# Performance work log

Hardware: AMD Instinct MI355X
Metric: run time of the kernel (lower is better)

## Reference

```python
import jax, jax.numpy as jnp
import numpy as np

N_PP = 100000   # papers
N_A = 50000     # authors
N_AP = N_PP + N_A
DIM = 16
B = 8192        # sampled node set sizes
E = 500000      # edges per modality
ALPHA = 0.5
EPS = 1e-12


def _cdist(x, y):
    # Euclidean cdist via quadratic expansion (avoids [N,M,d] intermediate)
    sq = (jnp.sum(x * x, -1)[:, None] + jnp.sum(y * y, -1)[None, :]
          - 2.0 * x @ y.T)
    return jnp.sqrt(jnp.maximum(sq, EPS))


def _pdist(x, y):
    d = x - y
    return jnp.sqrt(jnp.sum(d * d, -1) + EPS)


def setup_inputs() -> dict:
    key = jax.random.key(0)
    ks = jax.random.split(key, 10)
    u = lambda k, s: jax.random.uniform(k, s, jnp.float32, -1.0, 1.0)  # 2*rand-1
    p = u(ks[0], (N_PP, DIM))
    p_star = u(ks[1], (N_PP, DIM))
    a = u(ks[2], (N_A, DIM))
    beta_ap = u(ks[3], (N_AP,))
    gamma_pp = u(ks[4], (2 * N_PP,))
    edges_pp = jax.random.randint(ks[5], (2, E), 0, N_PP, jnp.int32)
    e_ap0 = jax.random.randint(ks[6], (1, E), 0, N_PP, jnp.int32)
    e_ap1 = jax.random.randint(ks[7], (1, E), N_PP, N_AP, jnp.int32)
    edges_ap = jnp.concatenate([e_ap0, e_ap1], 0)
    p_star_nodes = jnp.sort(jax.random.randint(ks[8], (B,), 0, N_PP, jnp.int32))
    kk = jax.random.split(ks[9], 2)
    p_nodes = jax.random.randint(kk[0], (B,), 0, N_PP, jnp.int32)
    a_nodes = jax.random.randint(kk[1], (B,), N_PP, N_AP, jnp.int32)
    return {"p": p, "p_star": p_star, "a": a, "beta_ap": beta_ap,
            "gamma_pp": gamma_pp, "edges_pp": edges_pp, "edges_ap": edges_ap,
            "p_star_nodes": p_star_nodes, "p_nodes": p_nodes, "a_nodes": a_nodes}


def reference(p, p_star, a, beta_ap, gamma_pp,
              edges_pp, edges_ap, p_star_nodes, p_nodes, a_nodes):
    # ---- pp modality ----
    # link term over edges (edges[0]=p_star idx, edges[1]=p idx)
    link_pp = jnp.sum(gamma_pp[edges_pp[0]] + gamma_pp[edges_pp[1] + N_PP]
                      - _pdist(p_star[edges_pp[0]], p[edges_pp[1]]))
    # non-link term: [B_pstar, B_p] matrix, upper-triangular (k=1) masked sum
    g_ps = gamma_pp[p_star_nodes]                 # [B]
    g_p = gamma_pp[p_nodes + N_PP]                # [B]
    mat_pp = g_ps[:, None] + g_p[None, :]         # == gamma_mat.T in torch code
    dist_pp = _cdist(p_star[p_star_nodes], p[p_nodes])
    nonlink_pp = jnp.sum(jnp.triu(jnp.exp(mat_pp - dist_pp), k=1))
    nll_pp = -(link_pp - nonlink_pp)

    # ---- ap modality ----
    link_ap = jnp.sum(beta_ap[edges_ap[0]] + beta_ap[edges_ap[1]]
                      - _pdist(p_star[edges_ap[0]], a[edges_ap[1] - N_PP]))
    b_ps = beta_ap[p_star_nodes]
    b_a = beta_ap[a_nodes]
    mat_ap = b_ps[:, None] + b_a[None, :]         # == beta_mat.T
    dist_ap = _cdist(p_star[p_star_nodes], a[a_nodes - N_PP])
    nonlink_ap = jnp.sum(jnp.exp(mat_ap - dist_ap))
    nll_ap = -(link_ap - nonlink_ap)

    # average batch loss as in __train_one_batch
    loss = ALPHA * nll_pp / B + (1.0 - ALPHA) * nll_ap / B
    return loss
```

## Files before the change

### kernel.cpp

```cpp
#include <hip/hip_runtime.h>

#define N_PP 100000
#define N_A  50000
#define N_AP 150000
#define NEDGE 500000
#define BSZ 8192
#define TILE 128
#define SCALE 1.44269504088896f
#define QSI4 (1.0f / 7.0f)

#define EB 977
#define GRID_P 2048
#define PP_JOBS 2080
#define AP_JOBS 4096
#define PJOBS (PP_JOBS + AP_JOBS)

#define GRID_FB 2048

typedef __attribute__((ext_vector_type(8)))  short bf16x8;
typedef __attribute__((ext_vector_type(16))) float f32x16;
typedef __attribute__((ext_vector_type(4)))  float f32x4;
typedef unsigned short u16;

#if __has_builtin(__builtin_amdgcn_sqrtf)
#define FAST_SQRT(x) __builtin_amdgcn_sqrtf(x)
#else
#define FAST_SQRT(x) sqrtf(x)
#endif
#if __has_builtin(__builtin_amdgcn_exp2f)
#define FAST_EXP2(x) __builtin_amdgcn_exp2f(x)
#else
#define FAST_EXP2(x) exp2f(x)
#endif

__device__ __forceinline__ u16 f2bf(float f) {
    unsigned u = __builtin_bit_cast(unsigned, f);
    u += 0x7FFFu + ((u >> 16) & 1u);
    return (u16)(u >> 16);
}
__device__ __forceinline__ float bf2f(u16 s) {
    unsigned u = ((unsigned)s) << 16;
    return __builtin_bit_cast(float, u);
}

__device__ __forceinline__ bf16x8 load_frag_f32(const float* __restrict__ src) {
    float4 v0 = *(const float4*)src;
    float4 v1 = *(const float4*)(src + 4);
    bf16x8 f;
    f[0] = (short)f2bf(v0.x); f[1] = (short)f2bf(v0.y);
    f[2] = (short)f2bf(v0.z); f[3] = (short)f2bf(v0.w);
    f[4] = (short)f2bf(v1.x); f[5] = (short)f2bf(v1.y);
    f[6] = (short)f2bf(v1.z); f[7] = (short)f2bf(v1.w);
    return f;
}

__device__ __forceinline__ float dist_i4q(int2 ra, int2 rb) {
    int d2 = 0;
#pragma unroll
    for (int c = 0; c < 8; ++c) {
        int va = (ra.x << (28 - 4 * c)) >> 28;
        int vb = (rb.x << (28 - 4 * c)) >> 28;
        int d = va - vb; d2 += d * d;
        int wa = (ra.y << (28 - 4 * c)) >> 28;
        int wb = (rb.y << (28 - 4 * c)) >> 28;
        int e = wa - wb; d2 += e * e;
    }
    return FAST_SQRT((float)d2) * QSI4;
}

__device__ __forceinline__ unsigned packq4x8(const float* __restrict__ v) {
    unsigned r = 0;
#pragma unroll
    for (int c = 0; c < 8; ++c) {
        int q = (int)rintf(v[c] * 7.0f);
        r |= ((unsigned)(q & 0xF)) << (4 * c);
    }
    return r;
}

__device__ __forceinline__ float pdist16_f32(const float* __restrict__ xv,
                                             const float* __restrict__ yv) {
    float d2 = 1e-12f;
#pragma unroll
    for (int c = 0; c < 16; c += 4) {
        float4 xq = *(const float4*)(xv + c);
        float4 yq = *(const float4*)(yv + c);
        float dx = xq.x - yq.x; d2 = fmaf(dx, dx, d2);
        float dy = xq.y - yq.y; d2 = fmaf(dy, dy, d2);
        float dz = xq.z - yq.z; d2 = fmaf(dz, dz, d2);
        float dw = xq.w - yq.w; d2 = fmaf(dw, dw, d2);
    }
    return sqrtf(d2);
}

__global__ __launch_bounds__(256) void prep_kernel(
        const float* __restrict__ p, const float* __restrict__ p_star,
        const float* __restrict__ a, const float* __restrict__ beta,
        const float* __restrict__ gamma,
        const int* __restrict__ psn, const int* __restrict__ pn,
        const int* __restrict__ an,
        int2* __restrict__ ps4, int2* __restrict__ p4, int2* __restrict__ a4,
        u16* __restrict__ gamma_h, u16* __restrict__ beta_h,
        u16* __restrict__ Xb, u16* __restrict__ Yp, u16* __restrict__ Ya,
        float* __restrict__ Xxx, float* __restrict__ Xg,
        float* __restrict__ Pyy, float* __restrict__ Pg,
        float* __restrict__ Ayy, float* __restrict__ Ag)
{
    const int NROWS = 250000;
    const int NBATCH = 3 * BSZ;
    const int NW = 2 * N_PP + N_AP;
    const int NITEMS = NROWS + NBATCH + NW;
    for (int i = blockIdx.x * 256 + threadIdx.x; i < NITEMS; i += gridDim.x * 256) {
        if (i < NROWS) {
            const float* src; int2* dst;
            if (i < 100000)      { src = p_star + (size_t)i * 16;       dst = ps4 + i; }
            else if (i < 200000) { src = p + (size_t)(i - 100000) * 16; dst = p4 + (i - 100000); }
            else                 { src = a + (size_t)(i - 200000) * 16; dst = a4 + (i - 200000); }
            float buf[16];
            *(float4*)(buf + 0)  = *(const float4*)(src + 0);
            *(float4*)(buf + 4)  = *(const float4*)(src + 4);
            *(float4*)(buf + 8)  = *(const float4*)(src + 8);
            *(float4*)(buf + 12) = *(const float4*)(src + 12);
            int2 q;
            q.x = (int)packq4x8(buf);
            q.y = (int)packq4x8(buf + 8);
            *dst = q;
        } else if (i < NROWS + NBATCH) {
            const int j = i - NROWS;
            const int which = j >> 13;
            const int r = j & (BSZ - 1);
            const float* src; float wsc; u16* drow; float* xxp; float* gp;
            if (which == 0) {
                int node = psn[r]; src = p_star + (size_t)node * 16;
                wsc = gamma[node] * SCALE; drow = Xb + (size_t)r * 16; xxp = Xxx; gp = Xg;
            } else if (which == 1) {
                int node = pn[r]; src = p + (size_t)node * 16;
                wsc = gamma[node + N_PP] * SCALE; drow = Yp + (size_t)r * 16; xxp = Pyy; gp = Pg;
            } else {
                int node = an[r]; src = a + (size_t)(node - N_PP) * 16;
                wsc = beta[node] * SCALE; drow = Ya + (size_t)r * 16; xxp = Ayy; gp = Ag;
            }
            bf16x8 lo = load_frag_f32(src);
            bf16x8 hi = load_frag_f32(src + 8);
            *(bf16x8*)drow = lo;
            *(bf16x8*)(drow + 8) = hi;
            float ss = 0.f;
#pragma unroll
            for (int c = 0; c < 8; ++c) {
                float q0 = bf2f((u16)lo[c]); ss = fmaf(q0, q0, ss);
                float q1 = bf2f((u16)hi[c]); ss = fmaf(q1, q1, ss);
            }
            xxp[r] = ss;
            gp[r] = wsc;
        } else {
            const int j = i - NROWS - NBATCH;
            if (j < 2 * N_PP) gamma_h[j] = f2bf(gamma[j]);
            else              beta_h[j - 2 * N_PP] = f2bf(beta[j - 2 * N_PP]);
        }
    }
}

template <bool DIAG>
__device__ __forceinline__ float epi_rt(
        const f32x16& ca, const f32x16& cb,
        const float* __restrict__ xxg, const float* __restrict__ gxg,
        int rb, float yy0, float gy0, float yy1, float gy1,
        int cj0, int cj1)
{
    f32x4 xxq[4], gxq[4];
#pragma unroll
    for (int q = 0; q < 4; ++q) {
        xxq[q] = *(const f32x4*)&xxg[rb + q * 8];
        gxq[q] = *(const f32x4*)&gxg[rb + q * 8];
    }
    float s = 0.f;
#pragma unroll
    for (int q = 0; q < 4; ++q) {
#pragma unroll
        for (int j = 0; j < 4; ++j) {
            const int reg = q * 4 + j;
            float sxy = xxq[q][j];
            float gx  = gxq[q][j];
            float sq0 = fmaf(-2.f, ca[reg], sxy + yy0);
            float d0  = FAST_SQRT(fmaxf(sq0, 1e-12f));
            float v0  = FAST_EXP2(fmaf(-SCALE, d0, gx + gy0));
            float sq1 = fmaf(-2.f, cb[reg], sxy + yy1);
            float d1  = FAST_SQRT(fmaxf(sq1, 1e-12f));
            float v1  = FAST_EXP2(fmaf(-SCALE, d1, gx + gy1));
            if (DIAG) {
                int row = rb + q * 8 + j;
                v0 = (cj0 > row) ? v0 : 0.f;
                v1 = (cj1 > row) ? v1 : 0.f;
            }
            s += v0 + v1;
        }
    }
    return s;
}

__device__ __forceinline__ void decode_job(int j, int& bx, int& by, bool& pp) {
    pp = (j < PP_JOBS);
    if (pp) {
        int k = j;
        float disc = sqrtf((float)(129 * 129 - 8 * k));
        by = (int)((129.0f - disc) * 0.5f);
        while (64 * by - (by * (by - 1)) / 2 > k) --by;
        while (64 * (by + 1) - ((by + 1) * by) / 2 <= k) ++by;
        bx = by + (k - (64 * by - (by * (by - 1)) / 2));
    } else {
        int k = j - PP_JOBS;
        bx = k & 63; by = k >> 6;
    }
}

__device__ __forceinline__ void load_pair_frags(
        int bx, int by, bool pp,
        const u16* __restrict__ Xb, const u16* __restrict__ Yp,
        const u16* __restrict__ Ya,
        int wr, int wc, int l31, int h,
        bf16x8& aF0, bf16x8& aF1, bf16x8& bF0, bf16x8& bF1)
{
    const u16* Ytab = pp ? Yp : Ya;
    const int ar0 = by * TILE + wr * 64 + l31;
    const int bc0 = bx * TILE + wc * 64 + l31;
    aF0 = *(const bf16x8*)(Xb   + (size_t)ar0 * 16 + h * 8);
    aF1 = *(const bf16x8*)(Xb   + (size_t)(ar0 + 32) * 16 + h * 8);
    bF0 = *(const bf16x8*)(Ytab + (size_t)bc0 * 16 + h * 8);
    bF1 = *(const bf16x8*)(Ytab + (size_t)(bc0 + 32) * 16 + h * 8);
}

__global__ __launch_bounds__(256) void work_kernel(
        const int* __restrict__ edges_pp, const int* __restrict__ edges_ap,
        const int2* __restrict__ ps4, const int2* __restrict__ p4,
        const int2* __restrict__ a4,
        const u16* __restrict__ gamma_h, const u16* __restrict__ beta_h,
        const u16* __restrict__ Xb, const u16* __restrict__ Yp,
        const u16* __restrict__ Ya,
        const float* __restrict__ Xxx, const float* __restrict__ Xg,
        const float* __restrict__ Pyy, const float* __restrict__ Pg,
        const float* __restrict__ Ayy, const float* __restrict__ Ag,
        float* __restrict__ epart, float* __restrict__ ppart)
{
    const int b = blockIdx.x;
    const int t = threadIdx.x;
    const int l = t & 63, w = t >> 6;

    if ((b % 3 == 0) && (b / 3 < EB)) {
        const int base = (b / 3) * 512;
        const int i0 = base + t;
        const int i1raw = base + 256 + t;
        const bool v1 = (i1raw < NEDGE);
        const int i1 = v1 ? i1raw : 0;

        int e0a = __builtin_nontemporal_load(edges_pp + i0);
        int e1a = __builtin_nontemporal_load(edges_pp + NEDGE + i0);
        int f0a = __builtin_nontemporal_load(edges_ap + i0);
        int f1a = __builtin_nontemporal_load(edges_ap + NEDGE + i0);
        int e0b = __builtin_nontemporal_load(edges_pp + i1);
        int e1b = __builtin_nontemporal_load(edges_pp + NEDGE + i1);
        int f0b = __builtin_nontemporal_load(edges_ap + i1);
        int f1b = __builtin_nontemporal_load(edges_ap + NEDGE + i1);

        int2 rA0 = ps4[e0a];
        int2 rA1 = p4[e1a];
        int2 rB0 = ps4[f0a];
        int2 rB1 = a4[f1a - N_PP];
        int2 rC0 = ps4[e0b];
        int2 rC1 = p4[e1b];
        int2 rD0 = ps4[f0b];
        int2 rD1 = a4[f1b - N_PP];
        float wA = bf2f(gamma_h[e0a]) + bf2f(gamma_h[e1a + N_PP]);
        float wB = bf2f(beta_h[f0a])  + bf2f(beta_h[f1a]);
        float wC = bf2f(gamma_h[e0b]) + bf2f(gamma_h[e1b + N_PP]);
        float wD = bf2f(beta_h[f0b])  + bf2f(beta_h[f1b]);

        float sppl = wA - dist_i4q(rA0, rA1);
        float sapl = wB - dist_i4q(rB0, rB1);
        float tpp2 = wC - dist_i4q(rC0, rC1);
        float tap2 = wD - dist_i4q(rD0, rD1);
        sppl += v1 ? tpp2 : 0.f;
        sapl += v1 ? tap2 : 0.f;

        __shared__ float rede[4][2];
#pragma unroll
        for (int o = 32; o > 0; o >>= 1) {
            sppl += __shfl_down(sppl, o, 64);
            sapl += __shfl_down(sapl, o, 64);
        }
        if (l == 0) { rede[w][0] = sppl; rede[w][1] = sapl; }
        __syncthreads();
        if (t < 2)
            epart[(size_t)(b / 3) * 2 + t] =
                rede[0][t] + rede[1][t] + rede[2][t] + rede[3][t];
        return;
    }

    const int pid = (b < 3 * EB) ? (b - b / 3 - 1) : (b - EB);

    const int wr = w >> 1, wc = w & 1;
    const int l31 = l & 31, h = l >> 5;
    const int cj0 = wc * 64 + l31, cj1 = cj0 + 32;
    const int rb0 = wr * 64 + 4 * h, rb1 = rb0 + 32;

    float s_ppn = 0.f, s_apn = 0.f;

    int j = pid;
    int bx, by; bool pp;
    bf16x8 aF0, aF1, bF0, bF1;
    if (j < PJOBS) {
        decode_job(j, bx, by, pp);
        load_pair_frags(bx, by, pp, Xb, Yp, Ya, wr, wc, l31, h, aF0, aF1, bF0, bF1);
    }

    while (j < PJOBS) {
        const int jn = j + GRID_P;
        int bxn, byn; bool ppn;
        bf16x8 nA0, nA1, nB0, nB1;
        const bool have_next = (jn < PJOBS);
        if (have_next) {
            decode_job(jn, bxn, byn, ppn);
            load_pair_frags(bxn, byn, ppn, Xb, Yp, Ya, wr, wc, l31, h, nA0, nA1, nB0, nB1);
        }

        const bool diag = pp && (bx == by);
        const float* yyP = (pp ? Pyy : Ayy) + bx * TILE;
        const float* gyP = (pp ? Pg  : Ag ) + bx * TILE;
        const float* xxg = Xxx + by * TILE;
        const float* gxg = Xg  + by * TILE;
        const float yy0 = yyP[cj0], gy0 = gyP[cj0];
        const float yy1 = yyP[cj1], gy1 = gyP[cj1];

        float sum;
        {
            f32x16 c0, c1;
#pragma unroll
            for (int i = 0; i < 16; ++i) { c0[i] = 0.f; c1[i] = 0.f; }
            c0 = __builtin_amdgcn_mfma_f32_32x32x16_bf16(aF0, bF0, c0, 0, 0, 0);
            c1 = __builtin_amdgcn_mfma_f32_32x32x16_bf16(aF0, bF1, c1, 0, 0, 0);
            sum = diag ? epi_rt<true >(c0, c1, xxg, gxg, rb0, yy0, gy0, yy1, gy1, cj0, cj1)
                       : epi_rt<false>(c0, c1, xxg, gxg, rb0, yy0, gy0, yy1, gy1, cj0, cj1);
        }
        {
            f32x16 c0, c1;
#pragma unroll
            for (int i = 0; i < 16; ++i) { c0[i] = 0.f; c1[i] = 0.f; }
            c0 = __builtin_amdgcn_mfma_f32_32x32x16_bf16(aF1, bF0, c0, 0, 0, 0);
            c1 = __builtin_amdgcn_mfma_f32_32x32x16_bf16(aF1, bF1, c1, 0, 0, 0);
            sum += diag ? epi_rt<true >(c0, c1, xxg, gxg, rb1, yy0, gy0, yy1, gy1, cj0, cj1)
                        : epi_rt<false>(c0, c1, xxg, gxg, rb1, yy0, gy0, yy1, gy1, cj0, cj1);
        }
        if (pp) s_ppn += sum; else s_apn += sum;

        j = jn;
        bx = bxn; by = byn; pp = ppn;
        aF0 = nA0; aF1 = nA1; bF0 = nB0; bF1 = nB1;
        if (!have_next) break;
    }

    __shared__ float redp[4][2];
#pragma unroll
    for (int o = 32; o > 0; o >>= 1) {
        s_ppn += __shfl_down(s_ppn, o, 64);
        s_apn += __shfl_down(s_apn, o, 64);
    }
    if (l == 0) { redp[w][0] = s_ppn; redp[w][1] = s_apn; }
    __syncthreads();
    if (t < 2)
        ppart[(size_t)pid * 2 + t] =
            redp[0][t] + redp[1][t] + redp[2][t] + redp[3][t];
}

__global__ __launch_bounds__(256) void finalize_split(
        const float* __restrict__ epart, const float* __restrict__ ppart,
        float* __restrict__ out)
{
    __shared__ double acc4[4];
    const int t = threadIdx.x;
    const int c = t >> 6, l = t & 63;
    double s = 0.0;
    if (c == 0)      { for (int i = l; i < EB; i += 64)     s += (double)epart[(size_t)i * 2 + 0]; }
    else if (c == 1) { for (int i = l; i < GRID_P; i += 64) s += (double)ppart[(size_t)i * 2 + 0]; }
    else if (c == 2) { for (int i = l; i < EB; i += 64)     s += (double)epart[(size_t)i * 2 + 1]; }
    else             { for (int i = l; i < GRID_P; i += 64) s += (double)ppart[(size_t)i * 2 + 1]; }
#pragma unroll
    for (int o = 32; o > 0; o >>= 1) s += __shfl_down(s, o, 64);
    if (l == 0) acc4[c] = s;
    __syncthreads();
    if (t == 0) {
        double nll_pp = -(acc4[0] - acc4[1]);
        double nll_ap = -(acc4[2] - acc4[3]);
        out[0] = (float)(0.5 * nll_pp / (double)BSZ + 0.5 * nll_ap / (double)BSZ);
    }
}

__global__ __launch_bounds__(256) void fused_fb(
        const float* __restrict__ p, const float* __restrict__ p_star,
        const float* __restrict__ a, const float* __restrict__ beta,
        const float* __restrict__ gamma,
        const int* __restrict__ edges_pp, const int* __restrict__ edges_ap,
        const int* __restrict__ psn, const int* __restrict__ pn,
        const int* __restrict__ an, float* __restrict__ partials)
{
    const int t = threadIdx.x;
    const int l = t & 63, w = t >> 6;
    const int wr = w >> 1, wc = w & 1;
    const int l31 = l & 31, h = l >> 5;

    __shared__ float sxx[TILE], sgx[TILE], syy[TILE], sgy[TILE];
    __shared__ float red4[4][4];

    float s_ppl = 0.f, s_ppn = 0.f, s_apl = 0.f, s_apn = 0.f;
    const int NJ = EB + PP_JOBS + AP_JOBS;

    for (int j = blockIdx.x; j < NJ; j += gridDim.x) {
        if (j < EB) {
            const int base = j * 512;
#pragma unroll
            for (int k = 0; k < 2; ++k) {
                int i = base + k * 256 + t;
                if (i < NEDGE) {
                    int e0 = edges_pp[i], e1 = edges_pp[NEDGE + i];
                    int f0 = edges_ap[i], f1 = edges_ap[NEDGE + i];
                    s_ppl += gamma[e0] + gamma[e1 + N_PP]
                           - pdist16_f32(p_star + (size_t)e0 * 16, p + (size_t)e1 * 16);
                    s_apl += beta[f0] + beta[f1]
                           - pdist16_f32(p_star + (size_t)f0 * 16, a + (size_t)(f1 - N_PP) * 16);
                }
            }
        } else {
            const bool pp = (j < EB + PP_JOBS);
            int bx, by;
            if (pp) {
                int k = j - EB;
                float disc = sqrtf((float)(129 * 129 - 8 * k));
                by = (int)((129.0f - disc) * 0.5f);
                while (64 * by - (by * (by - 1)) / 2 > k) --by;
                while (64 * (by + 1) - ((by + 1) * by) / 2 <= k) ++by;
                bx = by + (k - (64 * by - (by * (by - 1)) / 2));
            } else {
                int k = j - EB - PP_JOBS;
                bx = k & 63; by = k >> 6;
            }
            const bool diag = pp && (bx == by);
            const float* Y  = pp ? p : a;
            const float* wv = pp ? gamma : beta;
            const int* yn   = pp ? pn : an;
            const int wyo   = pp ? N_PP : 0;
            const int yvo   = pp ? 0 : -N_PP;
            const int ar0 = by * TILE + wr * 64 + l31;
            const int an0 = psn[ar0], an1 = psn[ar0 + 32];
            bf16x8 aF0 = load_frag_f32(p_star + (size_t)an0 * 16 + h * 8);
            bf16x8 aF1 = load_frag_f32(p_star + (size_t)an1 * 16 + h * 8);
            const int bc0g = bx * TILE + wc * 64 + l31;
            const int bn0 = yn[bc0g], bn1 = yn[bc0g + 32];
            bf16x8 bF0 = load_frag_f32(Y + (size_t)(bn0 + yvo) * 16 + h * 8);
            bf16x8 bF1 = load_frag_f32(Y + (size_t)(bn1 + yvo) * 16 + h * 8);
            {
                const bool isx = (t < 128);
                const int  r   = isx ? t : t - 128;
                const int  node = isx ? psn[by * TILE + r] : yn[bx * TILE + r];
                const float* src = isx ? (p_star + (size_t)node * 16)
                                       : (Y + (size_t)(node + yvo) * 16);
                float ss = 0.f;
#pragma unroll
                for (int c = 0; c < 16; c += 4) {
                    float4 v = *(const float4*)(src + c);
                    float q0 = bf2f(f2bf(v.x)), q1 = bf2f(f2bf(v.y));
                    float q2 = bf2f(f2bf(v.z)), q3 = bf2f(f2bf(v.w));
                    ss = fmaf(q0, q0, ss); ss = fmaf(q1, q1, ss);
                    ss = fmaf(q2, q2, ss); ss = fmaf(q3, q3, ss);
                }
                if (isx) { sxx[r] = ss; sgx[r] = wv[node] * SCALE; }
                else     { syy[r] = ss; sgy[r] = wv[node + wyo] * SCALE; }
            }
            __syncthreads();
            const int cj0 = wc * 64 + l31, cj1 = cj0 + 32;
            const float yy0 = syy[cj0], gy0 = sgy[cj0];
            const float yy1 = syy[cj1], gy1 = sgy[cj1];
            const int rb0 = wr * 64 + 4 * h, rb1 = rb0 + 32;

            f32x16 c00, c01, c10, c11;
#pragma unroll
            for (int i = 0; i < 16; ++i) { c00[i] = 0.f; c01[i] = 0.f; c10[i] = 0.f; c11[i] = 0.f; }
            c00 = __builtin_amdgcn_mfma_f32_32x32x16_bf16(aF0, bF0, c00, 0, 0, 0);
            c01 = __builtin_amdgcn_mfma_f32_32x32x16_bf16(aF0, bF1, c01, 0, 0, 0);
            c10 = __builtin_amdgcn_mfma_f32_32x32x16_bf16(aF1, bF0, c10, 0, 0, 0);
            c11 = __builtin_amdgcn_mfma_f32_32x32x16_bf16(aF1, bF1, c11, 0, 0, 0);

            float sum;
            if (diag) {
                sum = epi_rt<true >(c00, c01, sxx, sgx, rb0, yy0, gy0, yy1, gy1, cj0, cj1)
                    + epi_rt<true >(c10, c11, sxx, sgx, rb1, yy0, gy0, yy1, gy1, cj0, cj1);
            } else {
                sum = epi_rt<false>(c00, c01, sxx, sgx, rb0, yy0, gy0, yy1, gy1, cj0, cj1)
                    + epi_rt<false>(c10, c11, sxx, sgx, rb1, yy0, gy0, yy1, gy1, cj0, cj1);
            }
            if (pp) s_ppn += sum; else s_apn += sum;
            __syncthreads();
        }
    }

    float v4[4] = {s_ppl, s_ppn, s_apl, s_apn};
#pragma unroll
    for (int c = 0; c < 4; ++c) {
        float r = v4[c];
#pragma unroll
        for (int o = 32; o > 0; o >>= 1) r += __shfl_down(r, o, 64);
        if (l == 0) red4[w][c] = r;
    }
    __syncthreads();
    if (t < 4)
        partials[(size_t)blockIdx.x * 4 + t] =
            red4[0][t] + red4[1][t] + red4[2][t] + red4[3][t];
}

__global__ __launch_bounds__(256) void finalize_fb(
        const float* __restrict__ partials, float* __restrict__ out)
{
    __shared__ double acc4[4];
    const int t = threadIdx.x;
    const int c = t >> 6, l = t & 63;
    double s = 0.0;
    for (int i = l; i < GRID_FB; i += 64) s += (double)partials[(size_t)i * 4 + c];
#pragma unroll
    for (int o = 32; o > 0; o >>= 1) s += __shfl_down(s, o, 64);
    if (l == 0) acc4[c] = s;
    __syncthreads();
    if (t == 0) {
        double nll_pp = -(acc4[0] - acc4[1]);
        double nll_ap = -(acc4[2] - acc4[3]);
        out[0] = (float)(0.5 * nll_pp / (double)BSZ + 0.5 * nll_ap / (double)BSZ);
    }
}

extern "C" void kernel_launch(void* const* d_in, const int* in_sizes, int n_in,
                              void* d_out, int out_size, void* d_ws, size_t ws_size,
                              hipStream_t stream)
{
    const float* p       = (const float*)d_in[0];
    const float* p_star  = (const float*)d_in[1];
    const float* a       = (const float*)d_in[2];
    const float* beta    = (const float*)d_in[3];
    const float* gamma   = (const float*)d_in[4];
    const int* edges_pp  = (const int*)d_in[5];
    const int* edges_ap  = (const int*)d_in[6];
    const int* psn       = (const int*)d_in[7];
    const int* pn        = (const int*)d_in[8];
    const int* an        = (const int*)d_in[9];

    char* ws = (char*)d_ws;
    size_t off = 0;
    float* ppart = (float*)(ws + off); off += (size_t)GRID_P * 2 * sizeof(float);
    float* epart = (float*)(ws + off); off += (size_t)EB * 2 * sizeof(float);
    int2* ps4 = (int2*)(ws + off); off += (size_t)100000 * 8;
    int2* p4  = (int2*)(ws + off); off += (size_t)100000 * 8;
    int2* a4  = (int2*)(ws + off); off += (size_t)50000 * 8;
    u16* gamma_h = (u16*)(ws + off); off += (size_t)(2 * N_PP) * 2;
    u16* beta_h  = (u16*)(ws + off); off += (size_t)N_AP * 2;
    u16* Xb  = (u16*)(ws + off); off += (size_t)BSZ * 32;
    u16* Yp  = (u16*)(ws + off); off += (size_t)BSZ * 32;
    u16* Ya  = (u16*)(ws + off); off += (size_t)BSZ * 32;
    float* Xxx = (float*)(ws + off); off += BSZ * 4;
    float* Xg  = (float*)(ws + off); off += BSZ * 4;
    float* Pyy = (float*)(ws + off); off += BSZ * 4;
    float* Pg  = (float*)(ws + off); off += BSZ * 4;
    float* Ayy = (float*)(ws + off); off += BSZ * 4;
    float* Ag  = (float*)(ws + off); off += BSZ * 4;
    const bool packed = (ws_size >= off);

    if (packed) {
        prep_kernel<<<512, 256, 0, stream>>>(
            p, p_star, a, beta, gamma, psn, pn, an,
            ps4, p4, a4, gamma_h, beta_h,
            Xb, Yp, Ya, Xxx, Xg, Pyy, Pg, Ayy, Ag);
        work_kernel<<<EB + GRID_P, 256, 0, stream>>>(
            edges_pp, edges_ap, ps4, p4, a4, gamma_h, beta_h,
            Xb, Yp, Ya, Xxx, Xg, Pyy, Pg, Ayy, Ag, epart, ppart);
        finalize_split<<<1, 256, 0, stream>>>(epart, ppart, (float*)d_out);
    } else {
        float* fbpart = (float*)ws;
        fused_fb<<<GRID_FB, 256, 0, stream>>>(
            p, p_star, a, beta, gamma, edges_pp, edges_ap, psn, pn, an, fbpart);
        finalize_fb<<<1, 256, 0, stream>>>(fbpart, (float*)d_out);
    }
}
```

Measured before the change: 76.22 us.

## Merge edge-sum blocks into pairwise workers with a single 1024-block grid

Drops the separate edge-only blocks and has most of the 1024 persistent work blocks do one slice of the edge link sum before their pairwise MFMA jobs. Both results go through one combined four-value reduction per block. This removes 977 short-lived edge blocks and one reduction/sync pass per block, and halves the pairwise grid so each block runs about six jobs instead of three. In exchange, the edge gather latency now sits directly in front of the pairwise work in the same block, and the smaller grid may reduce latency hiding.

After: 71.29 us. -6.5%, faster.

```diff
diff --git a/kernel.cpp b/kernel.cpp
--- a/kernel.cpp
+++ b/kernel.cpp
@@ -10,7 +10,8 @@
 #define QSI4 (1.0f / 7.0f)
 
 #define EB 977
-#define GRID_P 2048
+#define GRID_W 1024
+#define EOFF 32
 #define PP_JOBS 2080
 #define AP_JOBS 4096
 #define PJOBS (PP_JOBS + AP_JOBS)
@@ -245,8 +246,11 @@
     const int t = threadIdx.x;
     const int l = t & 63, w = t >> 6;
 
-    if ((b % 3 == 0) && (b / 3 < EB)) {
-        const int base = (b / 3) * 512;
+    float s_ppl = 0.f, s_apl = 0.f;
+    const bool has_edge = (b >= EOFF) && (b < EOFF + EB);
+
+    if (has_edge) {
+        const int base = (b - EOFF) * 512;
         const int i0 = base + t;
         const int i1raw = base + 256 + t;
         const bool v1 = (i1raw < NEDGE);
@@ -274,28 +278,13 @@
         float wC = bf2f(gamma_h[e0b]) + bf2f(gamma_h[e1b + N_PP]);
         float wD = bf2f(beta_h[f0b])  + bf2f(beta_h[f1b]);
 
-        float sppl = wA - dist_i4q(rA0, rA1);
-        float sapl = wB - dist_i4q(rB0, rB1);
+        s_ppl = wA - dist_i4q(rA0, rA1);
+        s_apl = wB - dist_i4q(rB0, rB1);
         float tpp2 = wC - dist_i4q(rC0, rC1);
         float tap2 = wD - dist_i4q(rD0, rD1);
-        sppl += v1 ? tpp2 : 0.f;
-        sapl += v1 ? tap2 : 0.f;
-
-        __shared__ float rede[4][2];
-#pragma unroll
-        for (int o = 32; o > 0; o >>= 1) {
-            sppl += __shfl_down(sppl, o, 64);
-            sapl += __shfl_down(sapl, o, 64);
-        }
-        if (l == 0) { rede[w][0] = sppl; rede[w][1] = sapl; }
-        __syncthreads();
-        if (t < 2)
-            epart[(size_t)(b / 3) * 2 + t] =
-                rede[0][t] + rede[1][t] + rede[2][t] + rede[3][t];
-        return;
-    }
-
-    const int pid = (b < 3 * EB) ? (b - b / 3 - 1) : (b - EB);
+        s_ppl += v1 ? tpp2 : 0.f;
+        s_apl += v1 ? tap2 : 0.f;
+    }
 
     const int wr = w >> 1, wc = w & 1;
     const int l31 = l & 31, h = l >> 5;
@@ -304,7 +293,7 @@
 
     float s_ppn = 0.f, s_apn = 0.f;
 
-    int j = pid;
+    int j = b;
     int bx, by; bool pp;
     bf16x8 aF0, aF1, bF0, bF1;
     if (j < PJOBS) {
@@ -313,7 +302,7 @@
     }
 
     while (j < PJOBS) {
-        const int jn = j + GRID_P;
+        const int jn = j + GRID_W;
         int bxn, byn; bool ppn;
         bf16x8 nA0, nA1, nB0, nB1;
         const bool have_next = (jn < PJOBS);
@@ -357,17 +346,23 @@
         if (!have_next) break;
     }
 
-    __shared__ float redp[4][2];
-#pragma unroll
-    for (int o = 32; o > 0; o >>= 1) {
-        s_ppn += __shfl_down(s_ppn, o, 64);
-        s_apn += __shfl_down(s_apn, o, 64);
-    }
-    if (l == 0) { redp[w][0] = s_ppn; redp[w][1] = s_apn; }
+    __shared__ float red4[4][4];
+    float v4[4] = {s_ppl, s_ppn, s_apl, s_apn};
+#pragma unroll
+    for (int c = 0; c < 4; ++c) {
+        float r = v4[c];
+#pragma unroll
+        for (int o = 32; o > 0; o >>= 1) r += __shfl_down(r, o, 64);
+        if (l == 0) red4[w][c] = r;
+    }
     __syncthreads();
-    if (t < 2)
-        ppart[(size_t)pid * 2 + t] =
-            redp[0][t] + redp[1][t] + redp[2][t] + redp[3][t];
+    if (t < 2) {
+        if (has_edge)
+            epart[(size_t)(b - EOFF) * 2 + t] =
+                red4[0][2 * t] + red4[1][2 * t] + red4[2][2 * t] + red4[3][2 * t];
+        ppart[(size_t)b * 2 + t] =
+            red4[0][2 * t + 1] + red4[1][2 * t + 1] + red4[2][2 * t + 1] + red4[3][2 * t + 1];
+    }
 }
 
 __global__ __launch_bounds__(256) void finalize_split(
@@ -379,9 +374,9 @@
     const int c = t >> 6, l = t & 63;
     double s = 0.0;
     if (c == 0)      { for (int i = l; i < EB; i += 64)     s += (double)epart[(size_t)i * 2 + 0]; }
-    else if (c == 1) { for (int i = l; i < GRID_P; i += 64) s += (double)ppart[(size_t)i * 2 + 0]; }
+    else if (c == 1) { for (int i = l; i < GRID_W; i += 64) s += (double)ppart[(size_t)i * 2 + 0]; }
     else if (c == 2) { for (int i = l; i < EB; i += 64)     s += (double)epart[(size_t)i * 2 + 1]; }
-    else             { for (int i = l; i < GRID_P; i += 64) s += (double)ppart[(size_t)i * 2 + 1]; }
+    else             { for (int i = l; i < GRID_W; i += 64) s += (double)ppart[(size_t)i * 2 + 1]; }
 #pragma unroll
     for (int o = 32; o > 0; o >>= 1) s += __shfl_down(s, o, 64);
     if (l == 0) acc4[c] = s;
@@ -550,7 +545,7 @@
 
     char* ws = (char*)d_ws;
     size_t off = 0;
-    float* ppart = (float*)(ws + off); off += (size_t)GRID_P * 2 * sizeof(float);
+    float* ppart = (float*)(ws + off); off += (size_t)GRID_W * 2 * sizeof(float);
     float* epart = (float*)(ws + off); off += (size_t)EB * 2 * sizeof(float);
     int2* ps4 = (int2*)(ws + off); off += (size_t)100000 * 8;
     int2* p4  = (int2*)(ws + off); off += (size_t)100000 * 8;
@@ -573,7 +568,7 @@
             p, p_star, a, beta, gamma, psn, pn, an,
             ps4, p4, a4, gamma_h, beta_h,
             Xb, Yp, Ya, Xxx, Xg, Pyy, Pg, Ayy, Ag);
-        work_kernel<<<EB + GRID_P, 256, 0, stream>>>(
+        work_kernel<<<GRID_W, 256, 0, stream>>>(
             edges_pp, edges_ap, ps4, p4, a4, gamma_h, beta_h,
             Xb, Yp, Ya, Xxx, Xg, Pyy, Pg, Ayy, Ag, epart, ppart);
         finalize_split<<<1, 256, 0, stream>>>(epart, ppart, (float*)d_out);
```
